# Kernel tuning notes

Hardware: AMD Instinct MI355X
Metric: run time of the kernel (lower is better)

## Reference

```python
import jax, jax.numpy as jnp
import numpy as np

D_MODEL = 1024
NUM_HEADS = 16
NUM_KV_HEADS = 4
HEAD_DIM = D_MODEL // NUM_HEADS  # 64
KV_DIM = HEAD_DIM * NUM_KV_HEADS  # 256
B, N = 2, 2048


def setup_inputs() -> dict:
    key = jax.random.key(0)
    ks = jax.random.split(key, 7)
    std = 1.0 / np.sqrt(D_MODEL)
    return {
        "x": jax.random.normal(ks[0], (B, N, D_MODEL), dtype=jnp.float32),
        "cos": jax.random.uniform(ks[1], (N, HEAD_DIM // 2), dtype=jnp.float32),
        "sin": jax.random.uniform(ks[2], (N, HEAD_DIM // 2), dtype=jnp.float32),
        "Wq": jax.random.normal(ks[3], (D_MODEL, D_MODEL), dtype=jnp.float32) * std,
        "Wk": jax.random.normal(ks[4], (D_MODEL, KV_DIM), dtype=jnp.float32) * std,
        "Wv": jax.random.normal(ks[5], (D_MODEL, KV_DIM), dtype=jnp.float32) * std,
        "Wo": jax.random.normal(ks[6], (D_MODEL, D_MODEL), dtype=jnp.float32) * std,
    }


def _rope(t, cos, sin):
    # t: [B, H, N, head_dim]; cos/sin: [N, head_dim//2]
    t1, t2 = t[..., ::2], t[..., 1::2]
    c = cos[None, None]
    s = sin[None, None]
    # NOTE: halves are concatenated (not re-interleaved), faithful to source.
    return jnp.concatenate([t1 * c - t2 * s, t1 * s + t2 * c], axis=-1)


def reference(x, cos, sin, Wq, Wk, Wv, Wo):
    b, n, d = x.shape
    scale = HEAD_DIM ** -0.5
    q = (x @ Wq).reshape(b, n, NUM_HEADS, HEAD_DIM).transpose(0, 2, 1, 3)
    k = (x @ Wk).reshape(b, n, NUM_KV_HEADS, HEAD_DIM).transpose(0, 2, 1, 3)
    v = (x @ Wv).reshape(b, n, NUM_KV_HEADS, HEAD_DIM).transpose(0, 2, 1, 3)
    q = _rope(q, cos, sin)
    k = _rope(k, cos, sin)
    num_rep = NUM_HEADS // NUM_KV_HEADS
    k = jnp.repeat(k, num_rep, axis=1)  # [b, H, n, hd]
    v = jnp.repeat(v, num_rep, axis=1)
    attn = jnp.einsum("bhqd,bhkd->bhqk", q, k) * scale
    attn = jax.nn.softmax(attn, axis=-1)
    out = jnp.einsum("bhqk,bhkd->bhqd", attn, v)
    out = out.transpose(0, 2, 1, 3).reshape(b, n, d)
    return out @ Wo
```

## Files before the change

kernel.cpp:

```cpp
#include <hip/hip_runtime.h>
#include <math.h>

#define D_MODEL 1024
#define NHEADS  16
#define NKV     4
#define HDIM    64
#define KVDIM   256
#define BB      2
#define NN      2048
#define MROWS   (BB*NN)
#define QKVN    1536
#define NTASK   (MROWS*NHEADS)
#define NSPLIT  2
#define KVBLK   128
#define NTILE   ((NN/NSPLIT)/KVBLK)

typedef unsigned short ushort_t;
typedef unsigned int uint_t;
typedef float    f32x4 __attribute__((ext_vector_type(4)));
typedef _Float16 h16x8 __attribute__((ext_vector_type(8)));
typedef _Float16 h16x4 __attribute__((ext_vector_type(4)));
typedef __fp16   fp16x2 __attribute__((ext_vector_type(2)));

#define MFMAH(A,B,C)  __builtin_amdgcn_mfma_f32_16x16x32_f16((A),(B),(C),0,0,0)
#define MFMA16(A,B,C) __builtin_amdgcn_mfma_f32_16x16x16f16((A),(B),(C),0,0,0)
#define EXP2(x) __builtin_amdgcn_exp2f(x)

#define GLDS(gp, lp) __builtin_amdgcn_global_load_lds( \
    (const __attribute__((address_space(1))) void*)(gp), \
    (__attribute__((address_space(3))) void*)(lp), 16, 0, 0)

__device__ __forceinline__ ushort_t f2h(float f) {
    _Float16 h = (_Float16)f;
    return *(ushort_t*)&h;
}
__device__ __forceinline__ float h2f(ushort_t u) {
    return (float)(*(const _Float16*)&u);
}
__device__ __forceinline__ uint_t pk2h(float a, float b) {
    fp16x2 v = __builtin_amdgcn_cvt_pkrtz(a, b);
    return *(uint_t*)&v;
}

__global__ __launch_bounds__(256)
void prep_kernel(const float* __restrict__ x, const float* __restrict__ Wq,
                 const float* __restrict__ Wk, const float* __restrict__ Wv,
                 const float* __restrict__ Wo, ushort_t* __restrict__ xb,
                 ushort_t* __restrict__ WqkvT, ushort_t* __restrict__ WoT)
{
    __shared__ float T[32][33];
    int blk = blockIdx.x;
    if (blk < 4096) {
        const int i = blk * 256 + threadIdx.x;
        float4 v = ((const float4*)x)[i];
        uint2 o;
        o.x = pk2h(v.x, v.y);
        o.y = pk2h(v.z, v.w);
        ((uint2*)xb)[i] = o;
        return;
    }
    blk -= 4096;
    const float* src; ushort_t* dst; int N, bx, by;
    if (blk < 1024)      { src = Wq; dst = WqkvT;                            N = D_MODEL; bx = blk & 31; by = blk >> 5; }
    else if (blk < 1280) { blk -= 1024; src = Wk; dst = WqkvT + (size_t)1024 * D_MODEL; N = KVDIM; bx = blk & 7; by = blk >> 3; }
    else if (blk < 1536) { blk -= 1280; src = Wv; dst = WqkvT + (size_t)1280 * D_MODEL; N = KVDIM; bx = blk & 7; by = blk >> 3; }
    else                 { blk -= 1536; src = Wo; dst = WoT;                 N = D_MODEL; bx = blk & 31; by = blk >> 5; }
    const int tx = threadIdx.x & 31, ty = threadIdx.x >> 5;
    const int n0 = bx * 32, k0 = by * 32;
#pragma unroll
    for (int i = 0; i < 4; i++)
        T[ty + i * 8][tx] = src[(size_t)(k0 + ty + i * 8) * N + n0 + tx];
    __syncthreads();
#pragma unroll
    for (int i = 0; i < 4; i++)
        dst[(size_t)(n0 + ty + i * 8) * D_MODEL + k0 + tx] = f2h(T[tx][ty + i * 8]);
}

#define NKW (MROWS*NKV*32)
#define NKBLK (NKW / 256)
__global__ __launch_bounds__(256)
void ropevt_kernel(const ushort_t* __restrict__ QKVh, const float* __restrict__ Cos,
                   const float* __restrict__ Sin, ushort_t* __restrict__ Kb,
                   ushort_t* __restrict__ Vt)
{
    __shared__ ushort_t T[32][34];
    if (blockIdx.x >= NKBLK) {
        const int blk2 = blockIdx.x - NKBLK;
        const int bx = blk2 & 63, by = (blk2 >> 6) & 7, b = blk2 >> 9;
        const int tx = threadIdx.x & 31, ty = threadIdx.x >> 5;
        const int n0 = bx * 32, d0 = by * 32;
#pragma unroll
        for (int i = 0; i < 4; i++)
            T[ty + i * 8][tx] =
                QKVh[(size_t)(b * NN + n0 + ty + i * 8) * QKVN + 1280 + d0 + tx];
        __syncthreads();
#pragma unroll
        for (int i = 0; i < 4; i++)
            Vt[(size_t)(b * 256 + d0 + ty + i * 8) * NN + n0 + tx] = T[tx][ty + i * 8];
        return;
    }
    const int i2 = blockIdx.x * 256 + threadIdx.x;
    const int row = i2 >> 7, rem = i2 & 127;
    const int h = rem >> 5, j = rem & 31;
    const int b = row >> 11, n = row & (NN - 1);
    const uint_t pr = *(const uint_t*)&QKVh[(size_t)row * QKVN + 1024 + h * 64 + 2 * j];
    const float e = h2f((ushort_t)pr), o = h2f((ushort_t)(pr >> 16));
    const float c = Cos[n * 32 + j], s = Sin[n * 32 + j];
    ushort_t* dst = Kb + ((size_t)(b * 4 + h) * NN + n) * 64;
    dst[j]      = f2h(e * c - o * s);
    dst[j + 32] = f2h(e * s + o * c);
}

__global__ __launch_bounds__(256)
void gemm_qkv(const ushort_t* __restrict__ A, const ushort_t* __restrict__ Bt,
              ushort_t* __restrict__ C, int M, int N, int K)
{
    __shared__ ushort_t As[4][128 * 32];
    __shared__ ushort_t Bs[4][64 * 32];

    const int tid  = threadIdx.x;
    const int wave = tid >> 6, lane = tid & 63;
    const int quad = lane >> 4, l16 = lane & 15;
    const int rowBase = blockIdx.y * 128, colBase = blockIdx.x * 64;
    const int wm = (wave >> 1) * 64, wn = (wave & 1) * 32;

    f32x4 acc[4][2];
    const f32x4 zz = {0.f, 0.f, 0.f, 0.f};
#pragma unroll
    for (int i = 0; i < 4; i++)
#pragma unroll
        for (int j = 0; j < 2; j++) acc[i][j] = zz;

    const int sr = wave * 32 + (lane >> 2);
    const int sc = ((lane & 3) ^ ((lane >> 3) & 3)) * 8;
    const ushort_t* Ag0 = A + (size_t)(rowBase + sr) * K + sc;
    const ushort_t* Ag1 = A + (size_t)(rowBase + sr + 16) * K + sc;
    const int segA0 = (wave * 2 + 0) * 512, segA1 = (wave * 2 + 1) * 512;
    const int br = wave * 16 + (lane >> 2);
    const ushort_t* Bg0 = Bt + (size_t)(colBase + br) * K + sc;
    const int segB = wave * 512;

    const int fcol = (quad ^ ((l16 >> 1) & 3)) * 8;

    GLDS(Ag0, &As[0][segA0]);
    GLDS(Ag1, &As[0][segA1]);
    GLDS(Bg0, &Bs[0][segB]);
    GLDS(Ag0 + 32, &As[1][segA0]);
    GLDS(Ag1 + 32, &As[1][segA1]);
    GLDS(Bg0 + 32, &Bs[1][segB]);

#define QKV_COMPUTE(curslot) { \
        h16x8 af[4], bf[2]; \
        _Pragma("unroll") \
        for (int mt = 0; mt < 4; mt++) \
            af[mt] = *(const h16x8*)&As[curslot][(wm + mt * 16 + l16) * 32 + fcol]; \
        _Pragma("unroll") \
        for (int nt = 0; nt < 2; nt++) \
            bf[nt] = *(const h16x8*)&Bs[curslot][(wn + nt * 16 + l16) * 32 + fcol]; \
        _Pragma("unroll") \
        for (int mt = 0; mt < 4; mt++) \
            _Pragma("unroll") \
            for (int nt = 0; nt < 2; nt++) \
                acc[mt][nt] = MFMAH(af[mt], bf[nt], acc[mt][nt]); \
    }

    for (int k0 = 0; k0 < K; k0 += 64) {
        const int s0 = (k0 >> 5) & 3, s1 = (s0 + 1) & 3;
        const int s2 = (s0 + 2) & 3, s3 = (s0 + 3) & 3;
        __syncthreads();
        if (k0 + 64 < K) {
            GLDS(Ag0 + k0 + 64, &As[s2][segA0]);
            GLDS(Ag1 + k0 + 64, &As[s2][segA1]);
            GLDS(Bg0 + k0 + 64, &Bs[s2][segB]);
        }
        if (k0 + 96 < K) {
            GLDS(Ag0 + k0 + 96, &As[s3][segA0]);
            GLDS(Ag1 + k0 + 96, &As[s3][segA1]);
            GLDS(Bg0 + k0 + 96, &Bs[s3][segB]);
        }
        QKV_COMPUTE(s0);
        QKV_COMPUTE(s1);
    }
#undef QKV_COMPUTE

#pragma unroll
    for (int mt = 0; mt < 4; mt++)
#pragma unroll
        for (int nt = 0; nt < 2; nt++) {
            const int row = rowBase + wm + mt * 16 + quad * 4;
            const int col = colBase + wn + nt * 16 + l16;
#pragma unroll
            for (int r = 0; r < 4; r++)
                C[(size_t)(row + r) * N + col] = f2h(acc[mt][nt][r]);
        }
}

__global__ __launch_bounds__(256)
void attn_mfma(const ushort_t* __restrict__ QKVh, const float* __restrict__ Cos,
               const float* __restrict__ Sin, const ushort_t* __restrict__ Kb,
               const ushort_t* __restrict__ Vt, ushort_t* __restrict__ Pnum,
               float* __restrict__ Pl)
{
    const int qt = blockIdx.x, h = blockIdx.y;
    const int b = blockIdx.z >> 1, chunk = blockIdx.z & 1;
    const int kvh = h >> 2;
    const int tid = threadIdx.x;
    const int wave = tid >> 6, lane = tid & 63;
    const int quad = lane >> 4, l16 = lane & 15;

    __shared__ ushort_t Ks[2][128][64];
    __shared__ ushort_t Vs[2][64][128];

    const int row0 = qt * 256 + wave * 64;
    const float SC = 0.125f * 1.44269504f;

    h16x8 qf[4][2];
#pragma unroll
    for (int mt = 0; mt < 4; mt++) {
        const int n = row0 + mt * 16 + l16;
        const uint_t* pr =
            (const uint_t*)(QKVh + (size_t)(b * NN + n) * QKVN + h * 64) + quad * 8;
        uint4 pa = *(const uint4*)pr;
        uint4 pc = *(const uint4*)(pr + 4);
        const uint_t pk[8] = {pa.x, pa.y, pa.z, pa.w, pc.x, pc.y, pc.z, pc.w};
        const float4 c0 = *(const float4*)&Cos[(size_t)n * 32 + quad * 8];
        const float4 c1 = *(const float4*)&Cos[(size_t)n * 32 + quad * 8 + 4];
        const float4 s0 = *(const float4*)&Sin[(size_t)n * 32 + quad * 8];
        const float4 s1 = *(const float4*)&Sin[(size_t)n * 32 + quad * 8 + 4];
        const float cc[8] = {c0.x, c0.y, c0.z, c0.w, c1.x, c1.y, c1.z, c1.w};
        const float ss[8] = {s0.x, s0.y, s0.z, s0.w, s1.x, s1.y, s1.z, s1.w};
#pragma unroll
        for (int i = 0; i < 8; i++) {
            const float e = h2f((ushort_t)pk[i]);
            const float o = h2f((ushort_t)(pk[i] >> 16));
            qf[mt][0][i] = (_Float16)((e * cc[i] - o * ss[i]) * SC);
            qf[mt][1][i] = (_Float16)((e * ss[i] + o * cc[i]) * SC);
        }
    }

    h16x4 ones;
#pragma unroll
    for (int i = 0; i < 4; i++) ones[i] = (_Float16)1.0f;

    const ushort_t* kbase = Kb + (size_t)(b * 4 + kvh) * NN * 64;
    const ushort_t* vbase = Vt + (size_t)(b * 256 + kvh * 64) * NN;
    const int key_lo = chunk * (NN / NSPLIT);
    const int rot = (qt + ((h & 3) << 2)) & (NTILE - 1);

    const int krow = (wave << 3) + (lane >> 3);
    const int kseg = (lane & 7) ^ (krow & 7);
    const ushort_t* kp_lane = kbase + (size_t)krow * 64 + kseg * 8;
    const int vrow = (wave << 2) + (lane >> 4);
    const int vseg = (lane & 15) ^ (vrow & 7);
    const ushort_t* vp_lane = vbase + (size_t)vrow * NN + vseg * 8;

#define STAGE(key, bufidx) { \
        _Pragma("unroll") \
        for (int i = 0; i < 4; i++) { \
            GLDS(kp_lane + (size_t)((key) + i * 32) * 64, &Ks[bufidx][i * 32 + (wave << 3)][0]); \
            GLDS(vp_lane + (size_t)(i * 16) * NN + (key), &Vs[bufidx][i * 16 + (wave << 2)][0]); \
        } \
    }

    const f32x4 zz = {0.f, 0.f, 0.f, 0.f};
    f32x4 o[4][4];
#pragma unroll
    for (int mt = 0; mt < 4; mt++)
#pragma unroll
        for (int dt = 0; dt < 4; dt++) o[mt][dt] = zz;
    f32x4 lsum[4];
#pragma unroll
    for (int mt = 0; mt < 4; mt++) lsum[mt] = zz;

    STAGE(key_lo + rot * KVBLK, 0);

    const int kswz = l16 & 7;

    for (int t = 0; t < NTILE; t++) {
        const int cur = t & 1, nxt = cur ^ 1;
        __syncthreads();
        if (t < NTILE - 1) {
            const int kn = key_lo + ((rot + t + 1) & (NTILE - 1)) * KVBLK;
            STAGE(kn, nxt);
        }

#pragma unroll
        for (int kt = 0; kt < 8; kt++) {
            h16x8 kf0 = *(const h16x8*)&Ks[cur][kt * 16 + l16][(quad ^ kswz) << 3];
            h16x8 kf1 = *(const h16x8*)&Ks[cur][kt * 16 + l16][((4 + quad) ^ kswz) << 3];
            h16x4 va[4];
#pragma unroll
            for (int dt = 0; dt < 4; dt++)
                va[dt] = *(const h16x4*)&Vs[cur][dt * 16 + l16]
                    [(((kt * 2 + (quad >> 1)) ^ kswz) << 3) + ((quad & 1) << 2)];

            uint2 pb[4];
#pragma unroll
            for (int mt = 0; mt < 4; mt++) {
                f32x4 st = MFMAH(kf0, qf[mt][0], zz);
                st = MFMAH(kf1, qf[mt][1], st);
                pb[mt].x = pk2h(EXP2(st[0]), EXP2(st[1]));
                pb[mt].y = pk2h(EXP2(st[2]), EXP2(st[3]));
            }
#pragma unroll
            for (int mt = 0; mt < 4; mt++) {
                const h16x4 pbv = *(const h16x4*)&pb[mt];
#pragma unroll
                for (int dt = 0; dt < 4; dt++)
                    o[mt][dt] = MFMA16(va[dt], pbv, o[mt][dt]);
                lsum[mt] = MFMA16(ones, pbv, lsum[mt]);
            }
        }
    }
#undef STAGE

    const size_t task0 = (size_t)(b * 16 + h) * NN + row0;
    ushort_t* np = Pnum + ((size_t)chunk * NTASK + task0) * 64;
#pragma unroll
    for (int mt = 0; mt < 4; mt++) {
        const float lt = lsum[mt][0];
        const float inv = 1.0f / lt;
#pragma unroll
        for (int dt = 0; dt < 4; dt++) {
            f32x4 v = o[mt][dt];
            uint2 pk;
            pk.x = pk2h(v[0] * inv, v[1] * inv);
            pk.y = pk2h(v[2] * inv, v[3] * inv);
            *(uint2*)&np[(size_t)(mt * 16 + l16) * 64 + dt * 16 + quad * 4] = pk;
        }
        if (quad == 0)
            Pl[(size_t)chunk * NTASK + task0 + mt * 16 + l16] = lt;
    }
}

__global__ __launch_bounds__(256)
void combine_kernel(const ushort_t* __restrict__ Pnum, const float* __restrict__ Pl,
                    ushort_t* __restrict__ Ob)
{
    const uint_t i = blockIdx.x * 256 + threadIdx.x;
    const int row = i >> 7;
    const int g = i & 127;
    const int col0 = g * 8;
    const int h = col0 >> 6, d = col0 & 63;
    const int b = row >> 11, n = row & (NN - 1);
    const size_t task = ((size_t)(b * 16 + h) << 11) + n;

    float l[NSPLIT], tot = 0.f;
#pragma unroll
    for (int c = 0; c < NSPLIT; c++) { l[c] = Pl[(size_t)c * NTASK + task]; tot += l[c]; }
    const float inv = 1.f / tot;

    uint4 in[NSPLIT];
#pragma unroll
    for (int c = 0; c < NSPLIT; c++)
        in[c] = *(const uint4*)&Pnum[((size_t)c * NTASK + task) * 64 + d];

    uint4 out;
    uint_t* po = (uint_t*)&out;
#pragma unroll
    for (int j = 0; j < 4; j++) {
        float x = 0.f, y = 0.f;
#pragma unroll
        for (int c = 0; c < NSPLIT; c++) {
            const float w = l[c] * inv;
            fp16x2 u = *(const fp16x2*)&((const uint_t*)&in[c])[j];
            x += w * (float)u.x;
            y += w * (float)u.y;
        }
        po[j] = pk2h(x, y);
    }
    *(uint4*)&Ob[(size_t)row * D_MODEL + col0] = out;
}

__global__ __launch_bounds__(256)
void gemm_wo(const ushort_t* __restrict__ A, const ushort_t* __restrict__ Bt,
             float* __restrict__ C)
{
    __shared__ ushort_t As[4][128 * 32];
    __shared__ ushort_t Bs[4][64 * 32];

    const int tid  = threadIdx.x;
    const int wave = tid >> 6, lane = tid & 63;
    const int quad = lane >> 4, l16 = lane & 15;
    const int rowBase = blockIdx.y * 128, colBase = blockIdx.x * 64;
    const int wm = (wave >> 1) * 64, wn = (wave & 1) * 32;

    f32x4 acc[4][2];
    const f32x4 zz = {0.f, 0.f, 0.f, 0.f};
#pragma unroll
    for (int i = 0; i < 4; i++)
#pragma unroll
        for (int j = 0; j < 2; j++) acc[i][j] = zz;

    const int sr = wave * 32 + (lane >> 2);
    const int sc = ((lane & 3) ^ ((lane >> 3) & 3)) * 8;
    const ushort_t* Ag0 = A + (size_t)(rowBase + sr) * D_MODEL + sc;
    const ushort_t* Ag1 = A + (size_t)(rowBase + sr + 16) * D_MODEL + sc;
    const int segA0 = (wave * 2 + 0) * 512, segA1 = (wave * 2 + 1) * 512;
    const int br = wave * 16 + (lane >> 2);
    const ushort_t* Bg0 = Bt + (size_t)(colBase + br) * D_MODEL + sc;
    const int segB = wave * 512;

    const int fcol = (quad ^ ((l16 >> 1) & 3)) * 8;

    GLDS(Ag0, &As[0][segA0]);
    GLDS(Ag1, &As[0][segA1]);
    GLDS(Bg0, &Bs[0][segB]);
    GLDS(Ag0 + 32, &As[1][segA0]);
    GLDS(Ag1 + 32, &As[1][segA1]);
    GLDS(Bg0 + 32, &Bs[1][segB]);

#define WO_COMPUTE(curslot) { \
        h16x8 af[4], bf[2]; \
        _Pragma("unroll") \
        for (int mt = 0; mt < 4; mt++) \
            af[mt] = *(const h16x8*)&As[curslot][(wm + mt * 16 + l16) * 32 + fcol]; \
        _Pragma("unroll") \
        for (int nt = 0; nt < 2; nt++) \
            bf[nt] = *(const h16x8*)&Bs[curslot][(wn + nt * 16 + l16) * 32 + fcol]; \
        _Pragma("unroll") \
        for (int mt = 0; mt < 4; mt++) \
            _Pragma("unroll") \
            for (int nt = 0; nt < 2; nt++) \
                acc[mt][nt] = MFMAH(af[mt], bf[nt], acc[mt][nt]); \
    }

    for (int k0 = 0; k0 < D_MODEL; k0 += 64) {
        const int s0 = (k0 >> 5) & 3, s1 = (s0 + 1) & 3;
        const int s2 = (s0 + 2) & 3, s3 = (s0 + 3) & 3;
        __syncthreads();
        if (k0 + 64 < D_MODEL) {
            GLDS(Ag0 + k0 + 64, &As[s2][segA0]);
            GLDS(Ag1 + k0 + 64, &As[s2][segA1]);
            GLDS(Bg0 + k0 + 64, &Bs[s2][segB]);
        }
        if (k0 + 96 < D_MODEL) {
            GLDS(Ag0 + k0 + 96, &As[s3][segA0]);
            GLDS(Ag1 + k0 + 96, &As[s3][segA1]);
            GLDS(Bg0 + k0 + 96, &Bs[s3][segB]);
        }
        WO_COMPUTE(s0);
        WO_COMPUTE(s1);
    }
#undef WO_COMPUTE

#pragma unroll
    for (int mt = 0; mt < 4; mt++)
#pragma unroll
        for (int nt = 0; nt < 2; nt++) {
            const int row = rowBase + wm + mt * 16 + quad * 4;
            const int col = colBase + wn + nt * 16 + l16;
#pragma unroll
            for (int r = 0; r < 4; r++)
                C[(size_t)(row + r) * D_MODEL + col] = acc[mt][nt][r];
        }
}

extern "C" void kernel_launch(void* const* d_in, const int* in_sizes, int n_in,
                              void* d_out, int out_size, void* d_ws, size_t ws_size,
                              hipStream_t stream)
{
    const float* x    = (const float*)d_in[0];
    const float* cosp = (const float*)d_in[1];
    const float* sinp = (const float*)d_in[2];
    const float* Wq   = (const float*)d_in[3];
    const float* Wk   = (const float*)d_in[4];
    const float* Wv   = (const float*)d_in[5];
    const float* Wo   = (const float*)d_in[6];

    char* w = (char*)d_ws;
    ushort_t* xb     = (ushort_t*)w;                       w += (size_t)MROWS * D_MODEL * 2;
    ushort_t* WqkvT  = (ushort_t*)w;                       w += (size_t)QKVN * D_MODEL * 2;
    ushort_t* WoT    = (ushort_t*)w;                       w += (size_t)D_MODEL * D_MODEL * 2;
    ushort_t* QKVh   = (ushort_t*)w;                       w += (size_t)MROWS * QKVN * 2;
    ushort_t* Kbuf   = (ushort_t*)w;                       w += (size_t)MROWS * KVDIM * 2;
    ushort_t* Vt     = (ushort_t*)w;                       w += (size_t)MROWS * KVDIM * 2;
    ushort_t* Obuf   = (ushort_t*)w;                       w += (size_t)MROWS * D_MODEL * 2;
    ushort_t* Pnum   = (ushort_t*)w;                       w += (size_t)NSPLIT * NTASK * 64 * 2;
    float*    Pl     = (float*)w;

    prep_kernel<<<6656, 256, 0, stream>>>(x, Wq, Wk, Wv, Wo, xb, WqkvT, WoT);

    gemm_qkv<<<dim3(QKVN / 64, MROWS / 128), 256, 0, stream>>>(
        xb, WqkvT, QKVh, MROWS, QKVN, D_MODEL);

    ropevt_kernel<<<NKBLK + 1024, 256, 0, stream>>>(
        QKVh, cosp, sinp, Kbuf, Vt);

    attn_mfma<<<dim3(NN / 256, NHEADS, BB * NSPLIT), 256, 0, stream>>>(
        QKVh, cosp, sinp, Kbuf, Vt, Pnum, Pl);

    combine_kernel<<<(MROWS * D_MODEL / 8) / 256, 256, 0, stream>>>(
        Pnum, Pl, Obuf);

    gemm_wo<<<dim3(D_MODEL / 64, MROWS / 128), 256, 0, stream>>>(
        Obuf, WoT, (float*)d_out);
}
```

Baseline: 185.8 us.

## Fuse K RoPE and V transpose into QKV GEMM epilogue via permuted Wk columns

The separate ropevt kernel is removed. The QKV GEMM epilogue now applies RoPE to K and writes V transposed directly, with Q written to its own buffer. Wk columns are permuted in the prep kernel so that each 64-wide tile holds matching even/odd pairs in the accumulator registers needed for the rotation. This saves one launch and a full read/write pass over the K/V data. The epilogue stores become scattered and uncoalesced. Separately, s_setprio is raised around the PV MFMA block in attention.

```diff
diff --git a/kernel.cpp b/kernel.cpp
--- a/kernel.cpp
+++ b/kernel.cpp
@@ -60,9 +60,9 @@
         return;
     }
     blk -= 4096;
-    const float* src; ushort_t* dst; int N, bx, by;
+    const float* src; ushort_t* dst; int N, bx, by; int kperm = 0;
     if (blk < 1024)      { src = Wq; dst = WqkvT;                            N = D_MODEL; bx = blk & 31; by = blk >> 5; }
-    else if (blk < 1280) { blk -= 1024; src = Wk; dst = WqkvT + (size_t)1024 * D_MODEL; N = KVDIM; bx = blk & 7; by = blk >> 3; }
+    else if (blk < 1280) { blk -= 1024; src = Wk; dst = WqkvT + (size_t)1024 * D_MODEL; N = KVDIM; bx = blk & 7; by = blk >> 3; kperm = 1; }
     else if (blk < 1536) { blk -= 1280; src = Wv; dst = WqkvT + (size_t)1280 * D_MODEL; N = KVDIM; bx = blk & 7; by = blk >> 3; }
     else                 { blk -= 1536; src = Wo; dst = WoT;                 N = D_MODEL; bx = blk & 31; by = blk >> 5; }
     const int tx = threadIdx.x & 31, ty = threadIdx.x >> 5;
@@ -72,52 +72,28 @@
         T[ty + i * 8][tx] = src[(size_t)(k0 + ty + i * 8) * N + n0 + tx];
     __syncthreads();
 #pragma unroll
-    for (int i = 0; i < 4; i++)
-        dst[(size_t)(n0 + ty + i * 8) * D_MODEL + k0 + tx] = f2h(T[tx][ty + i * 8]);
-}
-
-#define NKW (MROWS*NKV*32)
-#define NKBLK (NKW / 256)
-__global__ __launch_bounds__(256)
-void ropevt_kernel(const ushort_t* __restrict__ QKVh, const float* __restrict__ Cos,
-                   const float* __restrict__ Sin, ushort_t* __restrict__ Kb,
-                   ushort_t* __restrict__ Vt)
-{
-    __shared__ ushort_t T[32][34];
-    if (blockIdx.x >= NKBLK) {
-        const int blk2 = blockIdx.x - NKBLK;
-        const int bx = blk2 & 63, by = (blk2 >> 6) & 7, b = blk2 >> 9;
-        const int tx = threadIdx.x & 31, ty = threadIdx.x >> 5;
-        const int n0 = bx * 32, d0 = by * 32;
-#pragma unroll
-        for (int i = 0; i < 4; i++)
-            T[ty + i * 8][tx] =
-                QKVh[(size_t)(b * NN + n0 + ty + i * 8) * QKVN + 1280 + d0 + tx];
-        __syncthreads();
-#pragma unroll
-        for (int i = 0; i < 4; i++)
-            Vt[(size_t)(b * 256 + d0 + ty + i * 8) * NN + n0 + tx] = T[tx][ty + i * 8];
-        return;
-    }
-    const int i2 = blockIdx.x * 256 + threadIdx.x;
-    const int row = i2 >> 7, rem = i2 & 127;
-    const int h = rem >> 5, j = rem & 31;
-    const int b = row >> 11, n = row & (NN - 1);
-    const uint_t pr = *(const uint_t*)&QKVh[(size_t)row * QKVN + 1024 + h * 64 + 2 * j];
-    const float e = h2f((ushort_t)pr), o = h2f((ushort_t)(pr >> 16));
-    const float c = Cos[n * 32 + j], s = Sin[n * 32 + j];
-    ushort_t* dst = Kb + ((size_t)(b * 4 + h) * NN + n) * 64;
-    dst[j]      = f2h(e * c - o * s);
-    dst[j + 32] = f2h(e * s + o * c);
+    for (int i = 0; i < 4; i++) {
+        int c = n0 + ty + i * 8;
+        if (kperm) {
+            const int hd = c >> 6, ch = c & 63;
+            const int j = ch >> 1, odd = ch & 1;
+            const int p = ((j < 16) ? j : j + 16) + odd * 16;
+            c = hd * 64 + p;
+        }
+        dst[(size_t)c * D_MODEL + k0 + tx] = f2h(T[tx][ty + i * 8]);
+    }
 }
 
 __global__ __launch_bounds__(256)
 void gemm_qkv(const ushort_t* __restrict__ A, const ushort_t* __restrict__ Bt,
-              ushort_t* __restrict__ C, int M, int N, int K)
+              const float* __restrict__ Cos, const float* __restrict__ Sin,
+              ushort_t* __restrict__ Qh, ushort_t* __restrict__ Kb,
+              ushort_t* __restrict__ Vt)
 {
     __shared__ ushort_t As[4][128 * 32];
     __shared__ ushort_t Bs[4][64 * 32];
 
+    const int K = D_MODEL;
     const int tid  = threadIdx.x;
     const int wave = tid >> 6, lane = tid & 63;
     const int quad = lane >> 4, l16 = lane & 15;
@@ -183,20 +159,55 @@
     }
 #undef QKV_COMPUTE
 
-#pragma unroll
-    for (int mt = 0; mt < 4; mt++)
-#pragma unroll
-        for (int nt = 0; nt < 2; nt++) {
-            const int row = rowBase + wm + mt * 16 + quad * 4;
-            const int col = colBase + wn + nt * 16 + l16;
-#pragma unroll
-            for (int r = 0; r < 4; r++)
-                C[(size_t)(row + r) * N + col] = f2h(acc[mt][nt][r]);
-        }
+    if (colBase < 1024) {
+#pragma unroll
+        for (int mt = 0; mt < 4; mt++)
+#pragma unroll
+            for (int nt = 0; nt < 2; nt++) {
+                const int row = rowBase + wm + mt * 16 + quad * 4;
+                const int col = colBase + wn + nt * 16 + l16;
+#pragma unroll
+                for (int r = 0; r < 4; r++)
+                    Qh[(size_t)(row + r) * D_MODEL + col] = f2h(acc[mt][nt][r]);
+            }
+    } else if (colBase < 1280) {
+        const int h = (colBase - 1024) >> 6;
+        const int p = wn + l16;
+        const int j = (p < 32) ? p : p - 16;
+#pragma unroll
+        for (int mt = 0; mt < 4; mt++) {
+            const int rowm = rowBase + wm + mt * 16 + quad * 4;
+            const int bb = rowm >> 11, nb = rowm & (NN - 1);
+            ushort_t* dstK = Kb + ((size_t)(bb * 4 + h) * NN) * 64;
+#pragma unroll
+            for (int r = 0; r < 4; r++) {
+                const int n = nb + r;
+                const float c = Cos[n * 32 + j], s = Sin[n * 32 + j];
+                const float e = acc[mt][0][r], o = acc[mt][1][r];
+                ushort_t* dk = dstK + (size_t)n * 64;
+                dk[j]      = f2h(e * c - o * s);
+                dk[j + 32] = f2h(e * s + o * c);
+            }
+        }
+    } else {
+        const int v0 = colBase - 1280;
+#pragma unroll
+        for (int mt = 0; mt < 4; mt++)
+#pragma unroll
+            for (int nt = 0; nt < 2; nt++) {
+                const int d = v0 + wn + nt * 16 + l16;
+                const int rowm = rowBase + wm + mt * 16 + quad * 4;
+                const int bb = rowm >> 11, nb = rowm & (NN - 1);
+                uint2 pk;
+                pk.x = pk2h(acc[mt][nt][0], acc[mt][nt][1]);
+                pk.y = pk2h(acc[mt][nt][2], acc[mt][nt][3]);
+                *(uint2*)&Vt[((size_t)(bb * 256 + d)) * NN + nb] = pk;
+            }
+    }
 }
 
 __global__ __launch_bounds__(256)
-void attn_mfma(const ushort_t* __restrict__ QKVh, const float* __restrict__ Cos,
+void attn_mfma(const ushort_t* __restrict__ Qh, const float* __restrict__ Cos,
                const float* __restrict__ Sin, const ushort_t* __restrict__ Kb,
                const ushort_t* __restrict__ Vt, ushort_t* __restrict__ Pnum,
                float* __restrict__ Pl)
@@ -219,7 +230,7 @@
     for (int mt = 0; mt < 4; mt++) {
         const int n = row0 + mt * 16 + l16;
         const uint_t* pr =
-            (const uint_t*)(QKVh + (size_t)(b * NN + n) * QKVN + h * 64) + quad * 8;
+            (const uint_t*)(Qh + (size_t)(b * NN + n) * D_MODEL + h * 64) + quad * 8;
         uint4 pa = *(const uint4*)pr;
         uint4 pc = *(const uint4*)(pr + 4);
         const uint_t pk[8] = {pa.x, pa.y, pa.z, pa.w, pc.x, pc.y, pc.z, pc.w};
@@ -302,6 +313,7 @@
                 pb[mt].x = pk2h(EXP2(st[0]), EXP2(st[1]));
                 pb[mt].y = pk2h(EXP2(st[2]), EXP2(st[3]));
             }
+            __builtin_amdgcn_s_setprio(1);
 #pragma unroll
             for (int mt = 0; mt < 4; mt++) {
                 const h16x4 pbv = *(const h16x4*)&pb[mt];
@@ -310,6 +322,7 @@
                     o[mt][dt] = MFMA16(va[dt], pbv, o[mt][dt]);
                 lsum[mt] = MFMA16(ones, pbv, lsum[mt]);
             }
+            __builtin_amdgcn_s_setprio(0);
         }
     }
 #undef STAGE
@@ -472,7 +485,7 @@
     ushort_t* xb     = (ushort_t*)w;                       w += (size_t)MROWS * D_MODEL * 2;
     ushort_t* WqkvT  = (ushort_t*)w;                       w += (size_t)QKVN * D_MODEL * 2;
     ushort_t* WoT    = (ushort_t*)w;                       w += (size_t)D_MODEL * D_MODEL * 2;
-    ushort_t* QKVh   = (ushort_t*)w;                       w += (size_t)MROWS * QKVN * 2;
+    ushort_t* Qh     = (ushort_t*)w;                       w += (size_t)MROWS * D_MODEL * 2;
     ushort_t* Kbuf   = (ushort_t*)w;                       w += (size_t)MROWS * KVDIM * 2;
     ushort_t* Vt     = (ushort_t*)w;                       w += (size_t)MROWS * KVDIM * 2;
     ushort_t* Obuf   = (ushort_t*)w;                       w += (size_t)MROWS * D_MODEL * 2;
@@ -482,13 +495,10 @@
     prep_kernel<<<6656, 256, 0, stream>>>(x, Wq, Wk, Wv, Wo, xb, WqkvT, WoT);
 
     gemm_qkv<<<dim3(QKVN / 64, MROWS / 128), 256, 0, stream>>>(
-        xb, WqkvT, QKVh, MROWS, QKVN, D_MODEL);
-
-    ropevt_kernel<<<NKBLK + 1024, 256, 0, stream>>>(
-        QKVh, cosp, sinp, Kbuf, Vt);
+        xb, WqkvT, cosp, sinp, Qh, Kbuf, Vt);
 
     attn_mfma<<<dim3(NN / 256, NHEADS, BB * NSPLIT), 256, 0, stream>>>(
-        QKVh, cosp, sinp, Kbuf, Vt, Pnum, Pl);
+        Qh, cosp, sinp, Kbuf, Vt, Pnum, Pl);
 
     combine_kernel<<<(MROWS * D_MODEL / 8) / 256, 256, 0, stream>>>(
         Pnum, Pl, Obuf);
```

Measured after the change: 185.9 us. Within noise of the previous version (+0.0%).
